# Optimization experiments

Hardware: AMD Instinct MI355X
Metric: run time of the kernel (lower is better)

The kernel has to match this reference:

```python
import jax, jax.numpy as jnp
import numpy as np
from jax import lax

ALPHA = 2.0
T_TAGS = 8  # number of distinct connects tags
ANCHOR_POS_FACTOR = jnp.array([1.0, 1.0], dtype=jnp.float32)
POS_FACTOR = [2.0, 1.0]  # [4,4,4,2,1][-2:]
NEG_FACTOR = [2.0, 1.0]


def setup_inputs() -> dict:
    key = jax.random.key(0)
    ks = jax.random.split(key, 10)
    B, A, M = 2, 2, 64
    Da, Db = 128, 64
    logits_a = jax.random.normal(ks[0], (B, A, Da, Da, Da), dtype=jnp.float32)
    logits_b = jax.random.normal(ks[1], (B, A, Db, Db, Db), dtype=jnp.float32)
    # GT prob maps: background labeled -1 (negmask), sparse positives labeled 1
    prob_a = jnp.where(jax.random.uniform(ks[2], (B, A, Da, Da, Da)) < 0.995, -1.0, 1.0).astype(jnp.float32)
    prob_b = jnp.where(jax.random.uniform(ks[3], (B, A, Db, Db, Db)) < 0.995, -1.0, 1.0).astype(jnp.float32)
    connects_a = jax.random.randint(ks[4], (B, A, Da, Da, Da), 0, T_TAGS, dtype=jnp.int32)
    connects_b = jax.random.randint(ks[5], (B, A, Db, Db, Db), 0, T_TAGS, dtype=jnp.int32)
    def make_coord(k, D):
        ka, kz = jax.random.split(k)
        anc = jax.random.randint(ka, (B, M, 1), 0, A, dtype=jnp.int32)
        sp = jax.random.randint(kz, (B, M, 3), 0, D, dtype=jnp.int32)
        c = jnp.concatenate([anc, sp], axis=-1)
        # pad last quarter of rows with -1 (invalid), as in the original padded coord lists
        c = c.at[:, 3 * M // 4:, :].set(-1)
        return c
    coord_a = make_coord(ks[6], Da)
    coord_b = make_coord(ks[7], Db)
    fnames = jnp.arange(B, dtype=jnp.float32)
    return {"logits_a": logits_a, "logits_b": logits_b, "prob_a": prob_a, "prob_b": prob_b,
            "connects_a": connects_a, "connects_b": connects_b,
            "coord_a": coord_a, "coord_b": coord_b, "fnames": fnames}


def _level_loss(logits, prob_gt, connects, coord, pos_f, neg_f):
    # ---- negative branch: sigmoid/logsigmoid elementwise + NMS maxpool mask ----
    prob = jax.nn.sigmoid(logits)
    nll = -jax.nn.log_sigmoid(-logits)  # -log(1 - sigmoid(logit))
    negmask = (prob_gt == -1.0).astype(logits.dtype)
    # max_pool3d kernel 3, stride 1, pad 1 over (D,H,W); anchors are channels
    pooled = lax.reduce_window(prob, -jnp.inf, lax.max,
                               (1, 1, 3, 3, 3), (1, 1, 1, 1, 1), 'SAME')
    max_filter = lax.stop_gradient((pooled == prob).astype(logits.dtype))
    negmask = negmask * max_filter
    w_neg = lax.stop_gradient(prob) ** ALPHA * negmask
    loss_neg = jnp.sum(nll * w_neg) * neg_f
    count_neg = jnp.sum(w_neg)
    wsum_neg = jnp.sum(w_neg) * neg_f

    # ---- positive branch: batched gather at coords (pad rows = -1) ----
    B, M, _ = coord.shape
    valid = coord[:, :, 0] > -1                       # [B, M]
    c = jnp.where(valid[..., None], coord, 0)         # safe indices
    b_idx = jnp.arange(B)[:, None]
    lp = logits[b_idx, c[..., 0], c[..., 1], c[..., 2], c[..., 3]]  # [B, M]
    pp = jax.nn.sigmoid(lp)
    w1 = (1.0 - lax.stop_gradient(pp)) ** ALPHA
    w2 = ANCHOR_POS_FACTOR[c[..., 0]]
    vf = valid.astype(logits.dtype)
    loss_pos = -jnp.sum(jax.nn.log_sigmoid(lp) * w1 * w2 * vf) * pos_f
    count_pos = jnp.sum(w1 * vf)
    wsum_pos = jnp.sum(w1 * w2 * vf) * pos_f

    # ---- connects-tag segment-min grouping (torch.unique + per-tag min) ----
    tags = connects[b_idx, c[..., 0], c[..., 1], c[..., 2], c[..., 3]]  # [B, M]
    seg = (jnp.arange(B, dtype=jnp.int32)[:, None] * T_TAGS + tags).reshape(-1)
    data = jnp.where(valid, w1, jnp.inf).reshape(-1)
    seg_min = jax.ops.segment_min(data, seg, num_segments=B * T_TAGS).reshape(B, T_TAGS)
    seg_min = jnp.where(jnp.isfinite(seg_min), seg_min, -1.0)  # absent tags -> -1 sentinel
    return loss_pos, loss_neg, count_pos, count_neg, wsum_pos, wsum_neg, seg_min


def reference(logits_a, logits_b, prob_a, prob_b, connects_a, connects_b, coord_a, coord_b, fnames):
    ra = _level_loss(logits_a, prob_a, connects_a, coord_a, POS_FACTOR[0], NEG_FACTOR[0])
    rb = _level_loss(logits_b, prob_b, connects_b, coord_b, POS_FACTOR[1], NEG_FACTOR[1])
    cls_loss_pos = ra[0] + rb[0]
    cls_loss_neg = ra[1] + rb[1]
    count_pos = ra[2] + rb[2]
    count_neg = ra[3] + rb[3]
    wsum_pos = ra[4] + rb[4]
    wsum_neg = ra[5] + rb[5]
    # pred_prob summary: per (level, sample, tag) min positive weight; fnames broadcast alongside
    pred_prob_min = jnp.stack([ra[6], rb[6]], axis=0)  # [2, B, T_TAGS]
    return (cls_loss_pos, cls_loss_neg, count_pos, count_neg, wsum_pos, wsum_neg, pred_prob_min)
```

## Files before the change

kernel.cpp:

```cpp
#include <hip/hip_runtime.h>
#include <math.h>


#define NBLK_A 512
#define NBLK_B 64
#define NBLK_TOTAL (NBLK_A + NBLK_B + 1)

using f4 = __attribute__((ext_vector_type(4))) float;

__device__ __forceinline__ float fmax3(float a, float b, float c) {
    return fmaxf(a, fmaxf(b, c));
}

__device__ __forceinline__ f4 fmax3v(f4 a, f4 b, f4 c) {
    f4 r;
    r.x = fmax3(a.x, b.x, c.x); r.y = fmax3(a.y, b.y, c.y);
    r.z = fmax3(a.z, b.z, c.z); r.w = fmax3(a.w, b.w, c.w);
    return r;
}

template <int XQ>
__device__ __forceinline__ void emit_row(
    const f4 zw0, const f4 zw1, const f4 zw2, const f4 c, const f4 g,
    int xq, float& loss, float& wsum)
{
    f4 cz = fmax3v(zw0, zw1, zw2);
    float lco = __shfl_up(cz.w, 1);   if (xq == 0)      lco = cz.x;
    float rco = __shfl_down(cz.x, 1); if (xq == XQ - 1) rco = cz.w;
    float ms[4] = {fmax3(lco, cz.x, cz.y), fmax3(cz.x, cz.y, cz.z),
                   fmax3(cz.y, cz.z, cz.w), fmax3(cz.z, cz.w, rco)};
    float cs[4] = {c.x, c.y, c.z, c.w};
    float gs[4] = {g.x, g.y, g.z, g.w};
#pragma unroll
    for (int k = 0; k < 4; ++k) {
        if (gs[k] == -1.0f && ms[k] == cs[k]) {
            float e = __expf(cs[k]);
            float u = __builtin_amdgcn_rcpf(1.0f + e);
            float sc = e * u;
            float wv = sc * sc;
            wsum += wv;
            loss += (-__logf(u)) * wv;
        }
    }
}

template <int D, int LOG2D, int XQ>
__device__ __forceinline__ void neg_march2(
    const float* __restrict__ logits, const float* __restrict__ gt,
    int vol, int z, int y0, int xq, float& loss, float& wsum)
{
    const int x0 = xq << 2;
    const float* vb = logits + (vol << (3 * LOG2D));
    const int zm = z > 0 ? z - 1 : 0;
    const int zq = z + 2 < D ? z + 2 : D - 1;
    const float* p0 = vb + (zm << (2 * LOG2D));
    const float* p1 = vb + (z << (2 * LOG2D));
    const float* p2 = vb + ((z + 1) << (2 * LOG2D));
    const float* p3 = vb + (zq << (2 * LOG2D));
    const float* g1 = gt + (vol << (3 * LOG2D)) + (z << (2 * LOG2D));
    const float* g2 = gt + (vol << (3 * LOG2D)) + ((z + 1) << (2 * LOG2D));

    f4 za[3], zb[3];
    f4 ca[2], cb[2];
    f4 ga[2], gb[2];

#pragma unroll
    for (int s = 0; s < 10; ++s) {
        int yy = y0 - 1 + s;
        yy = yy < 0 ? 0 : (yy > D - 1 ? D - 1 : yy);
        const int ro = (yy << LOG2D) + x0;
        f4 r0 = *(const f4*)(p0 + ro);
        f4 r1 = *(const f4*)(p1 + ro);
        f4 r2 = *(const f4*)(p2 + ro);
        f4 r3 = *(const f4*)(p3 + ro);
        if (s >= 1 && s <= 8) {
            ga[s & 1] = __builtin_nontemporal_load((const f4*)(g1 + ro));
            gb[s & 1] = __builtin_nontemporal_load((const f4*)(g2 + ro));
        }
        za[s % 3] = fmax3v(r0, r1, r2);
        zb[s % 3] = fmax3v(r1, r2, r3);
        ca[s & 1] = r1;
        cb[s & 1] = r2;
        if (s >= 2) {
            emit_row<XQ>(za[0], za[1], za[2], ca[(s - 1) & 1], ga[(s - 1) & 1],
                         xq, loss, wsum);
            emit_row<XQ>(zb[0], zb[1], zb[2], cb[(s - 1) & 1], gb[(s - 1) & 1],
                         xq, loss, wsum);
        }
    }
}

__global__ __launch_bounds__(256, 4) void fused_kernel(
    const float* __restrict__ la, const float* __restrict__ lb,
    const float* __restrict__ ga, const float* __restrict__ gb,
    const int* __restrict__ conn_a, const int* __restrict__ conn_b,
    const int* __restrict__ coord_a, const int* __restrict__ coord_b,
    float* __restrict__ ws, float* __restrict__ out)
{
    __shared__ float sred[8];
    __shared__ float w1s[128];
    __shared__ float tgf[128];
    const int bid = blockIdx.x;
    const int t = threadIdx.x;
    float loss = 0.0f, wsum = 0.0f;
    int accIdx = -1;

    if (bid < NBLK_A) {
        accIdx = 0;
        const int c = bid & 7;
        const int g = bid >> 3;
        const int yc = g & 15;
        const int vol = g >> 4;
        neg_march2<128, 7, 32>(la, ga, vol, c * 16 + (t >> 5) * 2, yc * 8,
                               t & 31, loss, wsum);
    } else if (bid < NBLK_A + NBLK_B) {
        accIdx = 2;
        const int b2 = bid - NBLK_A;
        const int c = b2 & 7;
        const int yc = b2 >> 3;
        const int vol = c >> 1;
        const int zg = c & 1;
        neg_march2<64, 6, 16>(lb, gb, vol, zg * 32 + (t >> 4) * 2, yc * 8,
                              t & 15, loss, wsum);
    } else {
        for (int level = 0; level < 2; ++level) {
            const float* logits = level ? lb : la;
            const int* conn = level ? conn_b : conn_a;
            const int* coord = level ? coord_b : coord_a;
            const int D = level ? 64 : 128;
            float li = 0.0f, ci = 0.0f;
            if (t < 128) {
                const int* c4 = coord + t * 4;
                int a = c4[0], zz = c4[1], yy = c4[2], xx = c4[3];
                bool valid = a > -1;
                int aa = valid ? a : 0, z2 = valid ? zz : 0,
                    y2 = valid ? yy : 0, x2 = valid ? xx : 0;
                int b = t >> 6;
                int off = (((b * 2 + aa) * D + z2) * D + y2) * D + x2;
                float lp = logits[off];
                int tag = conn[off];
                float s = 1.0f / (1.0f + expf(lp));
                float w1 = s * s;
                float vf = valid ? 1.0f : 0.0f;
                float sp = fmaxf(-lp, 0.0f) + log1pf(expf(-fabsf(lp)));
                li = sp * w1 * vf;
                ci = w1 * vf;
                w1s[t] = w1;
                tgf[t] = (float)(valid ? tag : -1);
            }
            for (int o = 32; o; o >>= 1) {
                li += __shfl_down(li, o);
                ci += __shfl_down(ci, o);
            }
            if ((t & 63) == 0) { sred[t >> 6] = li; sred[4 + (t >> 6)] = ci; }
            __syncthreads();
            if (t == 0) {
                atomicAdd(ws + 4 + 2 * level, sred[0] + sred[1] + sred[2] + sred[3]);
                atomicAdd(ws + 5 + 2 * level, sred[4] + sred[5] + sred[6] + sred[7]);
            }
            if (t < 16) {
                int bb = t >> 3, tg = t & 7;
                float mn = INFINITY;
                for (int i = 0; i < 64; ++i) {
                    int j = bb * 64 + i;
                    if (tgf[j] == (float)tg) mn = fminf(mn, w1s[j]);
                }
                out[6 + level * 16 + bb * 8 + tg] = isinf(mn) ? -1.0f : mn;
            }
            __syncthreads();
        }
    }

    if (accIdx >= 0) {
        for (int o = 32; o; o >>= 1) {
            loss += __shfl_down(loss, o);
            wsum += __shfl_down(wsum, o);
        }
        if ((t & 63) == 0) { sred[t >> 6] = loss; sred[4 + (t >> 6)] = wsum; }
        __syncthreads();
        if (t == 0) {
            float L = sred[0] + sred[1] + sred[2] + sred[3];
            float W = sred[4] + sred[5] + sred[6] + sred[7];
            if (L != 0.0f || W != 0.0f) {
                atomicAdd(ws + accIdx, L);
                atomicAdd(ws + accIdx + 1, W);
            }
        }
    }

    if (t == 0) {
        __threadfence();
        unsigned int old = atomicAdd((unsigned int*)(ws + 8), 1u);
        if (old == NBLK_TOTAL - 1) {
            float s0 = atomicAdd(ws + 0, 0.0f);
            float s1 = atomicAdd(ws + 1, 0.0f);
            float s2 = atomicAdd(ws + 2, 0.0f);
            float s3 = atomicAdd(ws + 3, 0.0f);
            float s4 = atomicAdd(ws + 4, 0.0f);
            float s5 = atomicAdd(ws + 5, 0.0f);
            float s6 = atomicAdd(ws + 6, 0.0f);
            float s7 = atomicAdd(ws + 7, 0.0f);
            out[0] = s4 * 2.0f + s6;
            out[1] = s0 * 2.0f + s2;
            out[2] = s5 + s7;
            out[3] = s1 + s3;
            out[4] = s5 * 2.0f + s7;
            out[5] = s1 * 2.0f + s3;
        }
    }
}

extern "C" void kernel_launch(void* const* d_in, const int* in_sizes, int n_in,
                              void* d_out, int out_size, void* d_ws, size_t ws_size,
                              hipStream_t stream) {
    const float* logits_a = (const float*)d_in[0];
    const float* logits_b = (const float*)d_in[1];
    const float* prob_a   = (const float*)d_in[2];
    const float* prob_b   = (const float*)d_in[3];
    const int*   conn_a   = (const int*)d_in[4];
    const int*   conn_b   = (const int*)d_in[5];
    const int*   coord_a  = (const int*)d_in[6];
    const int*   coord_b  = (const int*)d_in[7];
    float* out = (float*)d_out;
    float* ws  = (float*)d_ws;

    hipMemsetAsync(ws, 0, 12 * sizeof(float), stream);
    fused_kernel<<<NBLK_TOTAL, 256, 0, stream>>>(
        logits_a, logits_b, prob_a, prob_b,
        conn_a, conn_b, coord_a, coord_b, ws, out);
}
```

Baseline: 163.4 us.

## Share z-plane loads between partner lanes via shuffles and load GT only for NMS survivors

Each thread now loads three z-planes instead of four and gets the missing boundary plane from a partner lane (lane xor 32 or 16) through cross-lane shuffles. The goal is fewer redundant logits loads, since adjacent z-pairs overlap. The ground-truth row is now read only when at least one of the four voxels survives the max-pool equality test, which skips most prob reads. The cost is extra shuffle and select instructions, plus divergent GT loads that are no longer prefetched ahead of use, which can expose memory latency.

```diff
diff --git a/kernel.cpp b/kernel.cpp
--- a/kernel.cpp
+++ b/kernel.cpp
@@ -19,9 +19,23 @@
     return r;
 }
 
+__device__ __forceinline__ f4 selv(bool h, f4 a, f4 b) {
+    f4 r;
+    r.x = h ? a.x : b.x; r.y = h ? a.y : b.y;
+    r.z = h ? a.z : b.z; r.w = h ? a.w : b.w;
+    return r;
+}
+
+__device__ __forceinline__ f4 shflv(f4 v, int srcLane) {
+    f4 r;
+    r.x = __shfl(v.x, srcLane); r.y = __shfl(v.y, srcLane);
+    r.z = __shfl(v.z, srcLane); r.w = __shfl(v.w, srcLane);
+    return r;
+}
+
 template <int XQ>
 __device__ __forceinline__ void emit_row(
-    const f4 zw0, const f4 zw1, const f4 zw2, const f4 c, const f4 g,
+    const f4 zw0, const f4 zw1, const f4 zw2, const f4 c, const float* gp,
     int xq, float& loss, float& wsum)
 {
     f4 cz = fmax3v(zw0, zw1, zw2);
@@ -30,61 +44,68 @@
     float ms[4] = {fmax3(lco, cz.x, cz.y), fmax3(cz.x, cz.y, cz.z),
                    fmax3(cz.y, cz.z, cz.w), fmax3(cz.z, cz.w, rco)};
     float cs[4] = {c.x, c.y, c.z, c.w};
-    float gs[4] = {g.x, g.y, g.z, g.w};
+    bool mk[4] = {ms[0] == cs[0], ms[1] == cs[1], ms[2] == cs[2], ms[3] == cs[3]};
+    if (mk[0] | mk[1] | mk[2] | mk[3]) {
+        f4 g = __builtin_nontemporal_load((const f4*)gp);
+        float gs[4] = {g.x, g.y, g.z, g.w};
 #pragma unroll
-    for (int k = 0; k < 4; ++k) {
-        if (gs[k] == -1.0f && ms[k] == cs[k]) {
-            float e = __expf(cs[k]);
-            float u = __builtin_amdgcn_rcpf(1.0f + e);
-            float sc = e * u;
-            float wv = sc * sc;
-            wsum += wv;
-            loss += (-__logf(u)) * wv;
-        }
-    }
-}
-
-template <int D, int LOG2D, int XQ>
+        for (int k = 0; k < 4; ++k) {
+            if (mk[k] && gs[k] == -1.0f) {
+                float e = __expf(cs[k]);
+                float u = __builtin_amdgcn_rcpf(1.0f + e);
+                float sc = e * u;
+                float wv = sc * sc;
+                wsum += wv;
+                loss += (-__logf(u)) * wv;
+            }
+        }
+    }
+}
+
+template <int D, int LOG2D, int XQ, int PSH>
 __device__ __forceinline__ void neg_march2(
     const float* __restrict__ logits, const float* __restrict__ gt,
-    int vol, int z, int y0, int xq, float& loss, float& wsum)
+    int vol, int z, int y0, int xq, int h, int lane,
+    float& loss, float& wsum)
 {
     const int x0 = xq << 2;
     const float* vb = logits + (vol << (3 * LOG2D));
-    const int zm = z > 0 ? z - 1 : 0;
-    const int zq = z + 2 < D ? z + 2 : D - 1;
-    const float* p0 = vb + (zm << (2 * LOG2D));
-    const float* p1 = vb + (z << (2 * LOG2D));
-    const float* p2 = vb + ((z + 1) << (2 * LOG2D));
-    const float* p3 = vb + (zq << (2 * LOG2D));
-    const float* g1 = gt + (vol << (3 * LOG2D)) + (z << (2 * LOG2D));
-    const float* g2 = gt + (vol << (3 * LOG2D)) + ((z + 1) << (2 * LOG2D));
+    const int pa = h ? z : (z > 0 ? z - 1 : 0);
+    const int pb = h ? z + 1 : z;
+    const int pc = h ? (z + 2 < D ? z + 2 : D - 1) : z + 1;
+    const float* P0 = vb + (pa << (2 * LOG2D));
+    const float* P1 = vb + (pb << (2 * LOG2D));
+    const float* P2 = vb + (pc << (2 * LOG2D));
+    const float* g1 = gt + (vol << (3 * LOG2D)) + (z << (2 * LOG2D)) + x0;
+    const float* g2 = g1 + (1 << (2 * LOG2D));
+    const int partner = lane ^ PSH;
 
     f4 za[3], zb[3];
     f4 ca[2], cb[2];
-    f4 ga[2], gb[2];
 
 #pragma unroll
     for (int s = 0; s < 10; ++s) {
         int yy = y0 - 1 + s;
         yy = yy < 0 ? 0 : (yy > D - 1 ? D - 1 : yy);
         const int ro = (yy << LOG2D) + x0;
-        f4 r0 = *(const f4*)(p0 + ro);
-        f4 r1 = *(const f4*)(p1 + ro);
-        f4 r2 = *(const f4*)(p2 + ro);
-        f4 r3 = *(const f4*)(p3 + ro);
-        if (s >= 1 && s <= 8) {
-            ga[s & 1] = __builtin_nontemporal_load((const f4*)(g1 + ro));
-            gb[s & 1] = __builtin_nontemporal_load((const f4*)(g2 + ro));
-        }
-        za[s % 3] = fmax3v(r0, r1, r2);
-        zb[s % 3] = fmax3v(r1, r2, r3);
-        ca[s & 1] = r1;
-        cb[s & 1] = r2;
+        f4 r0 = *(const f4*)(P0 + ro);
+        f4 r1 = *(const f4*)(P1 + ro);
+        f4 r2 = *(const f4*)(P2 + ro);
+        f4 send = selv(h, r0, r2);
+        f4 recv = shflv(send, partner);
+        f4 q0 = selv(h, recv, r0);
+        f4 q1 = selv(h, r0, r1);
+        f4 q2 = selv(h, r1, r2);
+        f4 q3 = selv(h, r2, recv);
+        za[s % 3] = fmax3v(q0, q1, q2);
+        zb[s % 3] = fmax3v(q1, q2, q3);
+        ca[s & 1] = q1;
+        cb[s & 1] = q2;
         if (s >= 2) {
-            emit_row<XQ>(za[0], za[1], za[2], ca[(s - 1) & 1], ga[(s - 1) & 1],
+            const int yo = (y0 + s - 2) << LOG2D;
+            emit_row<XQ>(za[0], za[1], za[2], ca[(s - 1) & 1], g1 + yo,
                          xq, loss, wsum);
-            emit_row<XQ>(zb[0], zb[1], zb[2], cb[(s - 1) & 1], gb[(s - 1) & 1],
+            emit_row<XQ>(zb[0], zb[1], zb[2], cb[(s - 1) & 1], g2 + yo,
                          xq, loss, wsum);
         }
     }
@@ -102,6 +123,7 @@
     __shared__ float tgf[128];
     const int bid = blockIdx.x;
     const int t = threadIdx.x;
+    const int lane = t & 63;
     float loss = 0.0f, wsum = 0.0f;
     int accIdx = -1;
 
@@ -111,8 +133,8 @@
         const int g = bid >> 3;
         const int yc = g & 15;
         const int vol = g >> 4;
-        neg_march2<128, 7, 32>(la, ga, vol, c * 16 + (t >> 5) * 2, yc * 8,
-                               t & 31, loss, wsum);
+        neg_march2<128, 7, 32, 32>(la, ga, vol, c * 16 + (t >> 5) * 2, yc * 8,
+                                   t & 31, (t >> 5) & 1, lane, loss, wsum);
     } else if (bid < NBLK_A + NBLK_B) {
         accIdx = 2;
         const int b2 = bid - NBLK_A;
@@ -120,8 +142,8 @@
         const int yc = b2 >> 3;
         const int vol = c >> 1;
         const int zg = c & 1;
-        neg_march2<64, 6, 16>(lb, gb, vol, zg * 32 + (t >> 4) * 2, yc * 8,
-                              t & 15, loss, wsum);
+        neg_march2<64, 6, 16, 16>(lb, gb, vol, zg * 32 + (t >> 4) * 2, yc * 8,
+                                  t & 15, (t >> 4) & 1, lane, loss, wsum);
     } else {
         for (int level = 0; level < 2; ++level) {
             const float* logits = level ? lb : la;
```

After: 165.9 us. No clear change (+1.5%).

## March four z-planes per thread and halve block size to 128 threads

Applied to the files above, without the earlier changes.

Each thread now processes four consecutive z-planes per column sweep instead of two, loading six logit planes to produce four outputs. This cuts the redundant halo-plane reads from 2x to 1.5x per output. Blocks shrink to 128 threads so the grid size and coverage stay the same, and the reductions and the positive-branch code are adjusted to two wavefronts. Each thread holds more registers and there are fewer waves in flight to hide memory latency.

```diff
diff --git a/kernel.cpp b/kernel.cpp
--- a/kernel.cpp
+++ b/kernel.cpp
@@ -45,52 +45,61 @@
 }
 
 template <int D, int LOG2D, int XQ>
-__device__ __forceinline__ void neg_march2(
+__device__ __forceinline__ void neg_march4(
     const float* __restrict__ logits, const float* __restrict__ gt,
     int vol, int z, int y0, int xq, float& loss, float& wsum)
 {
     const int x0 = xq << 2;
     const float* vb = logits + (vol << (3 * LOG2D));
-    const int zm = z > 0 ? z - 1 : 0;
-    const int zq = z + 2 < D ? z + 2 : D - 1;
-    const float* p0 = vb + (zm << (2 * LOG2D));
-    const float* p1 = vb + (z << (2 * LOG2D));
-    const float* p2 = vb + ((z + 1) << (2 * LOG2D));
-    const float* p3 = vb + (zq << (2 * LOG2D));
-    const float* g1 = gt + (vol << (3 * LOG2D)) + (z << (2 * LOG2D));
-    const float* g2 = gt + (vol << (3 * LOG2D)) + ((z + 1) << (2 * LOG2D));
-
-    f4 za[3], zb[3];
-    f4 ca[2], cb[2];
-    f4 ga[2], gb[2];
+    const int pm = z > 0 ? z - 1 : 0;
+    const int pq = z + 4 < D ? z + 4 : D - 1;
+    const float* P0 = vb + (pm << (2 * LOG2D));
+    const float* P1 = vb + (z << (2 * LOG2D));
+    const float* P2 = vb + ((z + 1) << (2 * LOG2D));
+    const float* P3 = vb + ((z + 2) << (2 * LOG2D));
+    const float* P4 = vb + ((z + 3) << (2 * LOG2D));
+    const float* P5 = vb + (pq << (2 * LOG2D));
+    const float* gbase = gt + (vol << (3 * LOG2D)) + (z << (2 * LOG2D)) + x0;
+
+    f4 zf[4][3];
+    f4 cc[4][2];
+    f4 gg[4][2];
 
 #pragma unroll
     for (int s = 0; s < 10; ++s) {
         int yy = y0 - 1 + s;
         yy = yy < 0 ? 0 : (yy > D - 1 ? D - 1 : yy);
         const int ro = (yy << LOG2D) + x0;
-        f4 r0 = *(const f4*)(p0 + ro);
-        f4 r1 = *(const f4*)(p1 + ro);
-        f4 r2 = *(const f4*)(p2 + ro);
-        f4 r3 = *(const f4*)(p3 + ro);
+        f4 r0 = *(const f4*)(P0 + ro);
+        f4 r1 = *(const f4*)(P1 + ro);
+        f4 r2 = *(const f4*)(P2 + ro);
+        f4 r3 = *(const f4*)(P3 + ro);
+        f4 r4 = *(const f4*)(P4 + ro);
+        f4 r5 = *(const f4*)(P5 + ro);
         if (s >= 1 && s <= 8) {
-            ga[s & 1] = __builtin_nontemporal_load((const f4*)(g1 + ro));
-            gb[s & 1] = __builtin_nontemporal_load((const f4*)(g2 + ro));
-        }
-        za[s % 3] = fmax3v(r0, r1, r2);
-        zb[s % 3] = fmax3v(r1, r2, r3);
-        ca[s & 1] = r1;
-        cb[s & 1] = r2;
+            const int go = (y0 + s - 1) << LOG2D;
+#pragma unroll
+            for (int j = 0; j < 4; ++j)
+                gg[j][s & 1] = __builtin_nontemporal_load(
+                    (const f4*)(gbase + (j << (2 * LOG2D)) + go));
+        }
+        zf[0][s % 3] = fmax3v(r0, r1, r2);
+        zf[1][s % 3] = fmax3v(r1, r2, r3);
+        zf[2][s % 3] = fmax3v(r2, r3, r4);
+        zf[3][s % 3] = fmax3v(r3, r4, r5);
+        cc[0][s & 1] = r1; cc[1][s & 1] = r2;
+        cc[2][s & 1] = r3; cc[3][s & 1] = r4;
         if (s >= 2) {
-            emit_row<XQ>(za[0], za[1], za[2], ca[(s - 1) & 1], ga[(s - 1) & 1],
-                         xq, loss, wsum);
-            emit_row<XQ>(zb[0], zb[1], zb[2], cb[(s - 1) & 1], gb[(s - 1) & 1],
-                         xq, loss, wsum);
-        }
-    }
-}
-
-__global__ __launch_bounds__(256, 4) void fused_kernel(
+#pragma unroll
+            for (int j = 0; j < 4; ++j)
+                emit_row<XQ>(zf[j][0], zf[j][1], zf[j][2],
+                             cc[j][(s - 1) & 1], gg[j][(s - 1) & 1],
+                             xq, loss, wsum);
+        }
+    }
+}
+
+__global__ __launch_bounds__(128, 3) void fused_kernel(
     const float* __restrict__ la, const float* __restrict__ lb,
     const float* __restrict__ ga, const float* __restrict__ gb,
     const int* __restrict__ conn_a, const int* __restrict__ conn_b,
@@ -110,17 +119,20 @@
         const int c = bid & 7;
         const int g = bid >> 3;
         const int yc = g & 15;
-        const int vol = g >> 4;
-        neg_march2<128, 7, 32>(la, ga, vol, c * 16 + (t >> 5) * 2, yc * 8,
+        const int j = g >> 4;
+        const int unit = c * 4 + j;
+        const int vol = unit >> 3;
+        const int zg = unit & 7;
+        neg_march4<128, 7, 32>(la, ga, vol, zg * 16 + (t >> 5) * 4, yc * 8,
                                t & 31, loss, wsum);
     } else if (bid < NBLK_A + NBLK_B) {
         accIdx = 2;
         const int b2 = bid - NBLK_A;
         const int c = b2 & 7;
-        const int yc = b2 >> 3;
         const int vol = c >> 1;
         const int zg = c & 1;
-        neg_march2<64, 6, 16>(lb, gb, vol, zg * 32 + (t >> 4) * 2, yc * 8,
+        const int yc = b2 >> 3;
+        neg_march4<64, 6, 16>(lb, gb, vol, zg * 32 + (t >> 4) * 4, yc * 8,
                               t & 15, loss, wsum);
     } else {
         for (int level = 0; level < 2; ++level) {
@@ -128,26 +140,23 @@
             const int* conn = level ? conn_b : conn_a;
             const int* coord = level ? coord_b : coord_a;
             const int D = level ? 64 : 128;
-            float li = 0.0f, ci = 0.0f;
-            if (t < 128) {
-                const int* c4 = coord + t * 4;
-                int a = c4[0], zz = c4[1], yy = c4[2], xx = c4[3];
-                bool valid = a > -1;
-                int aa = valid ? a : 0, z2 = valid ? zz : 0,
-                    y2 = valid ? yy : 0, x2 = valid ? xx : 0;
-                int b = t >> 6;
-                int off = (((b * 2 + aa) * D + z2) * D + y2) * D + x2;
-                float lp = logits[off];
-                int tag = conn[off];
-                float s = 1.0f / (1.0f + expf(lp));
-                float w1 = s * s;
-                float vf = valid ? 1.0f : 0.0f;
-                float sp = fmaxf(-lp, 0.0f) + log1pf(expf(-fabsf(lp)));
-                li = sp * w1 * vf;
-                ci = w1 * vf;
-                w1s[t] = w1;
-                tgf[t] = (float)(valid ? tag : -1);
-            }
+            const int* c4 = coord + t * 4;
+            int a = c4[0], zz = c4[1], yy = c4[2], xx = c4[3];
+            bool valid = a > -1;
+            int aa = valid ? a : 0, z2 = valid ? zz : 0,
+                y2 = valid ? yy : 0, x2 = valid ? xx : 0;
+            int b = t >> 6;
+            int off = (((b * 2 + aa) * D + z2) * D + y2) * D + x2;
+            float lp = logits[off];
+            int tag = conn[off];
+            float s = 1.0f / (1.0f + expf(lp));
+            float w1 = s * s;
+            float vf = valid ? 1.0f : 0.0f;
+            float sp = fmaxf(-lp, 0.0f) + log1pf(expf(-fabsf(lp)));
+            float li = sp * w1 * vf;
+            float ci = w1 * vf;
+            w1s[t] = w1;
+            tgf[t] = (float)(valid ? tag : -1);
             for (int o = 32; o; o >>= 1) {
                 li += __shfl_down(li, o);
                 ci += __shfl_down(ci, o);
@@ -155,8 +164,8 @@
             if ((t & 63) == 0) { sred[t >> 6] = li; sred[4 + (t >> 6)] = ci; }
             __syncthreads();
             if (t == 0) {
-                atomicAdd(ws + 4 + 2 * level, sred[0] + sred[1] + sred[2] + sred[3]);
-                atomicAdd(ws + 5 + 2 * level, sred[4] + sred[5] + sred[6] + sred[7]);
+                atomicAdd(ws + 4 + 2 * level, sred[0] + sred[1]);
+                atomicAdd(ws + 5 + 2 * level, sred[4] + sred[5]);
             }
             if (t < 16) {
                 int bb = t >> 3, tg = t & 7;
@@ -179,8 +188,8 @@
         if ((t & 63) == 0) { sred[t >> 6] = loss; sred[4 + (t >> 6)] = wsum; }
         __syncthreads();
         if (t == 0) {
-            float L = sred[0] + sred[1] + sred[2] + sred[3];
-            float W = sred[4] + sred[5] + sred[6] + sred[7];
+            float L = sred[0] + sred[1];
+            float W = sred[4] + sred[5];
             if (L != 0.0f || W != 0.0f) {
                 atomicAdd(ws + accIdx, L);
                 atomicAdd(ws + accIdx + 1, W);
@@ -225,7 +234,7 @@
     float* ws  = (float*)d_ws;
 
     hipMemsetAsync(ws, 0, 12 * sizeof(float), stream);
-    fused_kernel<<<NBLK_TOTAL, 256, 0, stream>>>(
+    fused_kernel<<<NBLK_TOTAL, 128, 0, stream>>>(
         logits_a, logits_b, prob_a, prob_b,
         conn_a, conn_b, coord_a, coord_b, ws, out);
 }
```

Result: no change. 164.5 us (+0.7%).
